# Performance work log

Hardware: AMD Instinct MI355X
Metric: run time of the kernel (lower is better)

The kernel has to match this reference:

```python
import jax, jax.numpy as jnp
import numpy as np

N = 50000
E = 800000
IN_CH, CDK, EDGE_DIM = 40, 200, 10
HID, HEADS = 64, 4
NEG_SLOPE = 0.2
SM_EPS = 1e-16
BN_EPS = 1e-5


def _glorot(key, shape):
    fan = shape[0] + shape[-1]
    return jax.random.normal(key, shape, jnp.float32) * jnp.sqrt(2.0 / fan)


def setup_inputs() -> dict:
    key = jax.random.key(0)
    ks = iter(jax.random.split(key, 40))
    inp = {
        'x': jax.random.normal(next(ks), (N, IN_CH), jnp.float32),
        'cdk_desc': jax.random.normal(next(ks), (N, CDK), jnp.float32),
        'edge_src': jax.random.randint(next(ks), (E,), 0, N, jnp.int32),
        'edge_dst': jax.random.randint(next(ks), (E,), 0, N, jnp.int32),
        'edge_attr': jax.random.normal(next(ks), (E, EDGE_DIM), jnp.float32),
    }
    dims = [(IN_CH + CDK, HEADS, HID), (HID * HEADS, HEADS, HID), (HID * HEADS, 1, HID)]
    for i, (din, h, c) in enumerate(dims):
        inp[f'W{i}'] = _glorot(next(ks), (din, h * c))
        inp[f'as{i}'] = _glorot(next(ks), (h, c))
        inp[f'ad{i}'] = _glorot(next(ks), (h, c))
        inp[f'We{i}'] = _glorot(next(ks), (EDGE_DIM, h * c))
        inp[f'ae{i}'] = _glorot(next(ks), (h, c))
        inp[f'b{i}'] = jnp.zeros((h * c,), jnp.float32)
        inp[f'g{i}'] = jnp.ones((h * c,), jnp.float32)
        inp[f'be{i}'] = jnp.zeros((h * c,), jnp.float32)
    inp['linW'] = _glorot(next(ks), (HID, 1))
    inp['linB'] = jnp.zeros((1,), jnp.float32)
    return inp


def gat_conv(x, src, dst, ea, W, a_s, a_d, We, a_e, b, heads, c):
    # PyG GATConv: shared linear for src/dst, edge features, segment softmax.
    xp = (x @ W).reshape(N, heads, c)                 # [N,H,C]
    ep = (ea @ We).reshape(-1, heads, c)              # [Etot,H,C]
    al_s = (xp * a_s).sum(-1)                         # [N,H]
    al_d = (xp * a_d).sum(-1)                         # [N,H]
    al_e = (ep * a_e).sum(-1)                         # [Etot,H]
    alpha = jax.nn.leaky_relu(al_s[src] + al_d[dst] + al_e, NEG_SLOPE)
    m = jax.ops.segment_max(alpha, dst, num_segments=N)
    ex = jnp.exp(alpha - m[dst])
    den = jax.ops.segment_sum(ex, dst, num_segments=N)
    att = ex / (den[dst] + SM_EPS)                    # [Etot,H]
    out = jax.ops.segment_sum(xp[src] * att[:, :, None], dst, num_segments=N)
    return out.reshape(N, heads * c) + b


def batch_norm(x, g, be):
    mu = x.mean(0)
    var = x.var(0)
    return g * (x - mu) * jax.lax.rsqrt(var + BN_EPS) + be


def reference(x, cdk_desc, edge_src, edge_dst, edge_attr,
              W0, as0, ad0, We0, ae0, b0, g0, be0,
              W1, as1, ad1, We1, ae1, b1, g1, be1,
              W2, as2, ad2, We2, ae2, b2, g2, be2,
              linW, linB):
    # add self-loops once (PyG default add_self_loops=True, fill_value='mean')
    loop = jnp.arange(N, dtype=edge_src.dtype)
    src = jnp.concatenate([edge_src, loop])
    dst = jnp.concatenate([edge_dst, loop])
    ea_mean = edge_attr.mean(0)
    ea = jnp.concatenate([edge_attr, jnp.broadcast_to(ea_mean, (N, EDGE_DIM))], 0)

    h = jnp.concatenate([x, cdk_desc], axis=-1)
    layers = [
        (W0, as0, ad0, We0, ae0, b0, g0, be0, HEADS),
        (W1, as1, ad1, We1, ae1, b1, g1, be1, HEADS),
        (W2, as2, ad2, We2, ae2, b2, g2, be2, 1),
    ]
    for (W, a_s, a_d, We, a_e, b, g, be, heads) in layers:
        h = gat_conv(h, src, dst, ea, W, a_s, a_d, We, a_e, b, heads, HID)
        h = batch_norm(h, g, be)
        h = jax.nn.elu(h)
        # dropout is identity in eval mode
    out = h @ linW + linB
    return jax.nn.sigmoid(out).squeeze(-1)
```

## Files before the change

### kernel.cpp

```cpp
#include <hip/hip_runtime.h>
#include <math.h>

#define NNODES 50000
#define NEDGES 800000
#define ETOT   (NNODES + NEDGES)
#define EDIM   10
#define SMEPS  1e-16f
#define BNEPS  1e-5f
#define NSLOPE 0.2f

#define SCANB  ((NNODES + 255) / 256)

typedef _Float16 f16;
typedef f16 f16x8 __attribute__((ext_vector_type(8)));
typedef f16 f16x4 __attribute__((ext_vector_type(4)));
typedef float f32x4 __attribute__((ext_vector_type(4)));


__global__ void k_deg(const int* __restrict__ edst, int* __restrict__ deg) {
    int e = blockIdx.x * blockDim.x + threadIdx.x;
    if (e >= ETOT) return;
    int d = (e < NEDGES) ? edst[e] : (e - NEDGES);
    atomicAdd(&deg[d], 1);
}

__global__ void k_scan1(const int* __restrict__ deg, int* __restrict__ off,
                        int* __restrict__ partials) {
    __shared__ int sm[256];
    int t = threadIdx.x;
    int i = blockIdx.x * 256 + t;
    int v = (i < NNODES) ? deg[i] : 0;
    sm[t] = v;
    __syncthreads();
    int val = v;
    for (int d = 1; d < 256; d <<= 1) {
        int tv = (t >= d) ? sm[t - d] : 0;
        __syncthreads();
        val += tv;
        sm[t] = val;
        __syncthreads();
    }
    if (i < NNODES) off[i] = val - v;
    if (t == 255) partials[blockIdx.x] = val;
}

__global__ void k_scan2(int* __restrict__ partials, int* __restrict__ off) {
    __shared__ int sm[256];
    int t = threadIdx.x;
    int v = (t < SCANB) ? partials[t] : 0;
    sm[t] = v;
    __syncthreads();
    int val = v;
    for (int d = 1; d < 256; d <<= 1) {
        int tv = (t >= d) ? sm[t - d] : 0;
        __syncthreads();
        val += tv;
        sm[t] = val;
        __syncthreads();
    }
    if (t < SCANB) partials[t] = val - v;
    if (t == 255) off[NNODES] = ETOT;
}

__global__ void k_scan3(int* __restrict__ off, const int* __restrict__ partials) {
    int i = blockIdx.x * 256 + threadIdx.x;
    if (i < NNODES) off[i] += partials[blockIdx.x];
}

__global__ void k_scatter(const int* __restrict__ esrc, const int* __restrict__ edst,
                          const int* __restrict__ off, int* __restrict__ cursor,
                          int* __restrict__ csr_src, int* __restrict__ perm) {
    int e = blockIdx.x * blockDim.x + threadIdx.x;
    if (e >= ETOT) return;
    int s, d;
    if (e < NEDGES) { s = esrc[e]; d = edst[e]; }
    else            { s = d = e - NEDGES; }
    int pos  = atomicAdd(&cursor[d], 1);
    int slot = off[d] + pos;
    csr_src[slot] = s;
    perm[e] = slot;
}

__global__ void k_easum(const float* __restrict__ ea, float* __restrict__ easum) {
    float acc[EDIM];
#pragma unroll
    for (int d = 0; d < EDIM; ++d) acc[d] = 0.f;
    for (int r = blockIdx.x * blockDim.x + threadIdx.x; r < NEDGES;
         r += gridDim.x * blockDim.x) {
#pragma unroll
        for (int d = 0; d < EDIM; ++d) acc[d] += ea[r * EDIM + d];
    }
    __shared__ float sm[256];
    for (int d = 0; d < EDIM; ++d) {
        sm[threadIdx.x] = acc[d];
        __syncthreads();
        for (int s = 128; s > 0; s >>= 1) {
            if (threadIdx.x < s) sm[threadIdx.x] += sm[threadIdx.x + s];
            __syncthreads();
        }
        if (threadIdx.x == 0) atomicAdd(&easum[d], sm[0]);
        __syncthreads();
    }
}

__global__ void k_concat_h(const float* __restrict__ x, const float* __restrict__ cdk,
                           f16* __restrict__ out) {
    int i = blockIdx.x * blockDim.x + threadIdx.x;
    if (i >= NNODES * 256) return;
    int n = i >> 8, j = i & 255;
    float v = (j < 40) ? x[n * 40 + j] : (j < 240) ? cdk[n * 200 + (j - 40)] : 0.f;
    out[i] = (f16)v;
}

__global__ void k_wcvt(const float* __restrict__ W, f16* __restrict__ Wt,
                       int K, int NC) {
    int i = blockIdx.x * blockDim.x + threadIdx.x;
    if (i >= NC * 256) return;
    int n = i >> 8, k = i & 255;
    Wt[i] = (k < K) ? (f16)W[k * NC + n] : (f16)0.f;
}

#define GM_LDS 40
__global__ __launch_bounds__(256) void k_gemm_h(const f16* __restrict__ A,
                                                const f16* __restrict__ Bt,
                                                f16* __restrict__ C,
                                                int M, int NC) {
    __shared__ f16 As[128 * GM_LDS];
    __shared__ f16 Bs[64 * GM_LDS];
    const int t    = threadIdx.x;
    const int w    = t >> 6;
    const int lane = t & 63;
    const int row0 = blockIdx.x * 128;
    const int col0 = blockIdx.y * 64;

    const int ar = t >> 1;
    const int ak = (t & 1) * 16;
    const int bn = t >> 2;
    const int bk = (t & 3) * 8;

    const int l16 = lane & 15;
    const int kg  = lane >> 4;

    f32x4 acc[2][4];
#pragma unroll
    for (int i = 0; i < 2; ++i)
#pragma unroll
        for (int j = 0; j < 4; ++j) acc[i][j] = {0.f, 0.f, 0.f, 0.f};

    for (int k0 = 0; k0 < 256; k0 += 32) {
        f16x8 av0, av1;
#pragma unroll
        for (int i = 0; i < 8; ++i) { av0[i] = (f16)0.f; av1[i] = (f16)0.f; }
        if (row0 + ar < M) {
            const f16* ap = &A[(long)(row0 + ar) * 256 + k0 + ak];
            av0 = *(const f16x8*)ap;
            av1 = *(const f16x8*)(ap + 8);
        }
        *(f16x8*)&As[ar * GM_LDS + ak]     = av0;
        *(f16x8*)&As[ar * GM_LDS + ak + 8] = av1;
        f16x8 bv = *(const f16x8*)&Bt[(long)(col0 + bn) * 256 + k0 + bk];
        *(f16x8*)&Bs[bn * GM_LDS + bk] = bv;
        __syncthreads();

        f16x8 afr[2], bfr[4];
#pragma unroll
        for (int mi = 0; mi < 2; ++mi)
            afr[mi] = *(const f16x8*)&As[(w * 32 + mi * 16 + l16) * GM_LDS + kg * 8];
#pragma unroll
        for (int ni = 0; ni < 4; ++ni)
            bfr[ni] = *(const f16x8*)&Bs[(ni * 16 + l16) * GM_LDS + kg * 8];
#pragma unroll
        for (int mi = 0; mi < 2; ++mi)
#pragma unroll
            for (int ni = 0; ni < 4; ++ni)
                acc[mi][ni] = __builtin_amdgcn_mfma_f32_16x16x32_f16(
                    afr[mi], bfr[ni], acc[mi][ni], 0, 0, 0);
        __syncthreads();
    }
#pragma unroll
    for (int mi = 0; mi < 2; ++mi)
#pragma unroll
        for (int ni = 0; ni < 4; ++ni)
#pragma unroll
            for (int j = 0; j < 4; ++j) {
                int r = row0 + w * 32 + mi * 16 + kg * 4 + j;
                if (r < M) C[(long)r * NC + col0 + ni * 16 + l16] = (f16)acc[mi][ni][j];
            }
}

template <int H>
__global__ __launch_bounds__(256) void k_attn_node(const f16* __restrict__ xp,
                                                   const float* __restrict__ a_s,
                                                   const float* __restrict__ a_d,
                                                   float* __restrict__ als,
                                                   float* __restrict__ ald) {
    int gw   = (blockIdx.x * blockDim.x + threadIdx.x) >> 6;
    int lane = threadIdx.x & 63;
    if (gw >= NNODES) return;
    if constexpr (H == 4) {
        int h = lane >> 4, c4 = (lane & 15) * 4;
        f16x4 xh = *(const f16x4*)&xp[(long)gw * 256 + lane * 4];
        float4 xv = make_float4((float)xh[0], (float)xh[1], (float)xh[2], (float)xh[3]);
        float4 ws = *(const float4*)&a_s[h * 64 + c4];
        float4 wd = *(const float4*)&a_d[h * 64 + c4];
        float ps = xv.x * ws.x + xv.y * ws.y + xv.z * ws.z + xv.w * ws.w;
        float pd = xv.x * wd.x + xv.y * wd.y + xv.z * wd.z + xv.w * wd.w;
        for (int o = 1; o < 16; o <<= 1) { ps += __shfl_xor(ps, o); pd += __shfl_xor(pd, o); }
        if ((lane & 15) == 0) { als[gw * 4 + h] = ps; ald[gw * 4 + h] = pd; }
    } else {
        float xv = (float)xp[(long)gw * 64 + lane];
        float ps = xv * a_s[lane];
        float pd = xv * a_d[lane];
        for (int o = 1; o < 64; o <<= 1) { ps += __shfl_xor(ps, o); pd += __shfl_xor(pd, o); }
        if (lane == 0) { als[gw] = ps; ald[gw] = pd; }
    }
}

__global__ void k_ve_all(const float* __restrict__ We0, const float* __restrict__ ae0,
                         const float* __restrict__ We1, const float* __restrict__ ae1,
                         const float* __restrict__ We2, const float* __restrict__ ae2,
                         const float* __restrict__ easum,
                         float* __restrict__ VeAll, float* __restrict__ laAll) {
    int l = blockIdx.x;
    const float* We = (l == 0) ? We0 : (l == 1) ? We1 : We2;
    const float* ae = (l == 0) ? ae0 : (l == 1) ? ae1 : ae2;
    int H = (l == 2) ? 1 : 4;
    float* Ve = VeAll + l * 48;
    float* la = laAll + l * 4;
    int t = threadIdx.x;
    if (t < EDIM * H) {
        int d = t / H, h = t % H;
        float s = 0.f;
        for (int c = 0; c < 64; ++c) s += We[d * (H * 64) + h * 64 + c] * ae[h * 64 + c];
        Ve[d * H + h] = s;
    }
    __syncthreads();
    if (t < H) {
        float s = 0.f;
        for (int d = 0; d < EDIM; ++d) s += (easum[d] * (1.0f / NEDGES)) * Ve[d * H + t];
        la[t] = s;
    }
}

template <int H>
__global__ void k_edge(const float* __restrict__ ea, const int* __restrict__ esrc,
                       const int* __restrict__ edst, const float* __restrict__ als,
                       const float* __restrict__ ald, const float* __restrict__ Ve,
                       const float* __restrict__ loop_al, const int* __restrict__ perm,
                       float* __restrict__ alpha) {
    int e = blockIdx.x * blockDim.x + threadIdx.x;
    if (e >= ETOT) return;
    int s, d;
    float ale[H];
    if (e < NEDGES) {
        s = esrc[e]; d = edst[e];
#pragma unroll
        for (int h = 0; h < H; ++h) ale[h] = 0.f;
#pragma unroll
        for (int dd = 0; dd < EDIM; ++dd) {
            float v = ea[(long)e * EDIM + dd];
#pragma unroll
            for (int h = 0; h < H; ++h) ale[h] = fmaf(v, Ve[dd * H + h], ale[h]);
        }
    } else {
        s = d = e - NEDGES;
#pragma unroll
        for (int h = 0; h < H; ++h) ale[h] = loop_al[h];
    }
    int slot = perm[e];
#pragma unroll
    for (int h = 0; h < H; ++h) {
        float a = als[s * H + h] + ald[d * H + h] + ale[h];
        a = (a > 0.f) ? a : NSLOPE * a;
        alpha[(long)slot * H + h] = a;
    }
}

template <int H>
__global__ __launch_bounds__(256) void k_agg(const f16* __restrict__ xp,
                                             const float* __restrict__ alpha,
                                             const int* __restrict__ off,
                                             const int* __restrict__ csr_src,
                                             float* __restrict__ out) {
    int gw   = (blockIdx.x * blockDim.x + threadIdx.x) >> 6;
    int lane = threadIdx.x & 63;
    if (gw >= NNODES) return;
    int o0 = off[gw], o1 = off[gw + 1];

    if constexpr (H == 4) {
        constexpr int T = 4;
        int h  = lane >> 4;
        int il = lane & 15;
        int glane = lane & 48;

        float av[T];
        int   idx[T];
        float mx = -INFINITY;
#pragma unroll
        for (int t = 0; t < T; ++t) {
            int s = o0 + t * 16 + il;
            bool ok = (s < o1);
            float a = ok ? alpha[(long)s * 4 + h] : -INFINITY;
            idx[t] = ok ? csr_src[s] : 0;
            av[t] = a;
            mx = fmaxf(mx, a);
        }
        for (int s = o0 + T * 16 + il; s < o1; s += 16)
            mx = fmaxf(mx, alpha[(long)s * 4 + h]);
#pragma unroll
        for (int o = 1; o < 16; o <<= 1) mx = fmaxf(mx, __shfl_xor(mx, o));

        float den = 0.f;
#pragma unroll
        for (int t = 0; t < T; ++t) {
            float e = expf(av[t] - mx);
            av[t] = e;
            den += e;
        }
        for (int s = o0 + T * 16 + il; s < o1; s += 16)
            den += expf(alpha[(long)s * 4 + h] - mx);
#pragma unroll
        for (int o = 1; o < 16; o <<= 1) den += __shfl_xor(den, o);
        float di = 1.0f / (den + SMEPS);

        float4 acc0 = make_float4(0.f, 0.f, 0.f, 0.f);
        float4 acc1 = make_float4(0.f, 0.f, 0.f, 0.f);
#pragma unroll
        for (int t = 0; t < T; ++t) {
            int base = o0 + t * 16;
            if (base >= o1) break;
            int cnt = min(16, o1 - base);
            int j = 0;
            for (; j + 4 <= cnt; j += 4) {
                float w0 = __shfl(av[t],  glane + j,     64);
                int  sn0 = __shfl(idx[t], glane + j,     64);
                float w1 = __shfl(av[t],  glane + j + 1, 64);
                int  sn1 = __shfl(idx[t], glane + j + 1, 64);
                float w2 = __shfl(av[t],  glane + j + 2, 64);
                int  sn2 = __shfl(idx[t], glane + j + 2, 64);
                float w3 = __shfl(av[t],  glane + j + 3, 64);
                int  sn3 = __shfl(idx[t], glane + j + 3, 64);
                f16x4 x0 = *(const f16x4*)&xp[(long)sn0 * 256 + lane * 4];
                f16x4 x1 = *(const f16x4*)&xp[(long)sn1 * 256 + lane * 4];
                f16x4 x2 = *(const f16x4*)&xp[(long)sn2 * 256 + lane * 4];
                f16x4 x3 = *(const f16x4*)&xp[(long)sn3 * 256 + lane * 4];
                acc0.x = fmaf(w0, (float)x0[0], acc0.x);
                acc0.y = fmaf(w0, (float)x0[1], acc0.y);
                acc0.z = fmaf(w0, (float)x0[2], acc0.z);
                acc0.w = fmaf(w0, (float)x0[3], acc0.w);
                acc1.x = fmaf(w1, (float)x1[0], acc1.x);
                acc1.y = fmaf(w1, (float)x1[1], acc1.y);
                acc1.z = fmaf(w1, (float)x1[2], acc1.z);
                acc1.w = fmaf(w1, (float)x1[3], acc1.w);
                acc0.x = fmaf(w2, (float)x2[0], acc0.x);
                acc0.y = fmaf(w2, (float)x2[1], acc0.y);
                acc0.z = fmaf(w2, (float)x2[2], acc0.z);
                acc0.w = fmaf(w2, (float)x2[3], acc0.w);
                acc1.x = fmaf(w3, (float)x3[0], acc1.x);
                acc1.y = fmaf(w3, (float)x3[1], acc1.y);
                acc1.z = fmaf(w3, (float)x3[2], acc1.z);
                acc1.w = fmaf(w3, (float)x3[3], acc1.w);
            }
            for (; j < cnt; ++j) {
                float w  = __shfl(av[t],  glane + j, 64);
                int   sn = __shfl(idx[t], glane + j, 64);
                f16x4 xh = *(const f16x4*)&xp[(long)sn * 256 + lane * 4];
                acc0.x = fmaf(w, (float)xh[0], acc0.x);
                acc0.y = fmaf(w, (float)xh[1], acc0.y);
                acc0.z = fmaf(w, (float)xh[2], acc0.z);
                acc0.w = fmaf(w, (float)xh[3], acc0.w);
            }
        }
        for (int s = o0 + T * 16; s < o1; ++s) {
            float w  = expf(alpha[(long)s * 4 + h] - mx);
            int   sn = csr_src[s];
            f16x4 xh = *(const f16x4*)&xp[(long)sn * 256 + lane * 4];
            acc0.x = fmaf(w, (float)xh[0], acc0.x);
            acc0.y = fmaf(w, (float)xh[1], acc0.y);
            acc0.z = fmaf(w, (float)xh[2], acc0.z);
            acc0.w = fmaf(w, (float)xh[3], acc0.w);
        }
        float4 acc = make_float4((acc0.x + acc1.x) * di, (acc0.y + acc1.y) * di,
                                 (acc0.z + acc1.z) * di, (acc0.w + acc1.w) * di);
        *(float4*)&out[(long)gw * 256 + lane * 4] = acc;
    } else {
        constexpr int T = 2;
        float av[T];
        int   idx[T];
        float mx = -INFINITY;
#pragma unroll
        for (int t = 0; t < T; ++t) {
            int s = o0 + t * 64 + lane;
            bool ok = (s < o1);
            float a = ok ? alpha[s] : -INFINITY;
            idx[t] = ok ? csr_src[s] : 0;
            av[t] = a;
            mx = fmaxf(mx, a);
        }
        for (int s = o0 + T * 64 + lane; s < o1; s += 64)
            mx = fmaxf(mx, alpha[s]);
#pragma unroll
        for (int o = 1; o < 64; o <<= 1) mx = fmaxf(mx, __shfl_xor(mx, o));

        float den = 0.f;
#pragma unroll
        for (int t = 0; t < T; ++t) {
            float e = expf(av[t] - mx);
            av[t] = e;
            den += e;
        }
        for (int s = o0 + T * 64 + lane; s < o1; s += 64)
            den += expf(alpha[s] - mx);
#pragma unroll
        for (int o = 1; o < 64; o <<= 1) den += __shfl_xor(den, o);
        float di = 1.0f / (den + SMEPS);

        float acc0 = 0.f, acc1 = 0.f;
#pragma unroll
        for (int t = 0; t < T; ++t) {
            int base = o0 + t * 64;
            if (base >= o1) break;
            int cnt = min(64, o1 - base);
            int j = 0;
            for (; j + 4 <= cnt; j += 4) {
                float w0 = __shfl(av[t],  j,     64);
                int  sn0 = __shfl(idx[t], j,     64);
                float w1 = __shfl(av[t],  j + 1, 64);
                int  sn1 = __shfl(idx[t], j + 1, 64);
                float w2 = __shfl(av[t],  j + 2, 64);
                int  sn2 = __shfl(idx[t], j + 2, 64);
                float w3 = __shfl(av[t],  j + 3, 64);
                int  sn3 = __shfl(idx[t], j + 3, 64);
                float x0 = (float)xp[(long)sn0 * 64 + lane];
                float x1 = (float)xp[(long)sn1 * 64 + lane];
                float x2 = (float)xp[(long)sn2 * 64 + lane];
                float x3 = (float)xp[(long)sn3 * 64 + lane];
                acc0 = fmaf(w0, x0, acc0);
                acc1 = fmaf(w1, x1, acc1);
                acc0 = fmaf(w2, x2, acc0);
                acc1 = fmaf(w3, x3, acc1);
            }
            for (; j < cnt; ++j) {
                float w  = __shfl(av[t],  j, 64);
                int   sn = __shfl(idx[t], j, 64);
                acc0 = fmaf(w, (float)xp[(long)sn * 64 + lane], acc0);
            }
        }
        for (int s = o0 + T * 64; s < o1; ++s) {
            float w  = expf(alpha[s] - mx);
            int   sn = csr_src[s];
            acc0 = fmaf(w, (float)xp[(long)sn * 64 + lane], acc0);
        }
        out[(long)gw * 64 + lane] = (acc0 + acc1) * di;
    }
}

__global__ void k_bnstats(const float* __restrict__ x, int width,
                          float* __restrict__ s1, float* __restrict__ s2) {
    int col  = threadIdx.x % width;
    int rsub = threadIdx.x / width;
    int rpb  = 256 / width;
    float a = 0.f, b = 0.f;
    for (int r = blockIdx.x * rpb + rsub; r < NNODES; r += gridDim.x * rpb) {
        float v = x[(long)r * width + col];
        a += v; b += v * v;
    }
    atomicAdd(&s1[col], a);
    atomicAdd(&s2[col], b);
}

__global__ void k_bnfin(const float* __restrict__ s1, const float* __restrict__ s2,
                        const float* __restrict__ g, const float* __restrict__ be,
                        int width, float* __restrict__ scale, float* __restrict__ shift) {
    int c = blockIdx.x * blockDim.x + threadIdx.x;
    if (c >= width) return;
    float mu  = s1[c] * (1.0f / NNODES);
    float var = s2[c] * (1.0f / NNODES) - mu * mu;
    float sc  = g[c] * rsqrtf(var + BNEPS);
    scale[c] = sc;
    shift[c] = be[c] - mu * sc;
}

__global__ void k_bnelu_h(const float* __restrict__ xin, f16* __restrict__ xout,
                          const float* __restrict__ scale, const float* __restrict__ shift,
                          int width) {
    long i = (long)(blockIdx.x * blockDim.x + threadIdx.x);
    long total = (long)NNODES * width;
    if (i * 4 >= total) return;
    float4 v = *(const float4*)&xin[i * 4];
    int c = (int)((i * 4) % width);
    float4 sc = *(const float4*)&scale[c];
    float4 sh = *(const float4*)&shift[c];
    float y0 = v.x * sc.x + sh.x;
    float y1 = v.y * sc.y + sh.y;
    float y2 = v.z * sc.z + sh.z;
    float y3 = v.w * sc.w + sh.w;
    y0 = (y0 > 0.f) ? y0 : expm1f(y0);
    y1 = (y1 > 0.f) ? y1 : expm1f(y1);
    y2 = (y2 > 0.f) ? y2 : expm1f(y2);
    y3 = (y3 > 0.f) ? y3 : expm1f(y3);
    f16x4 o = {(f16)y0, (f16)y1, (f16)y2, (f16)y3};
    *(f16x4*)&xout[i * 4] = o;
}

__global__ __launch_bounds__(256) void k_final(const f16* __restrict__ h,
                                               const float* __restrict__ linW,
                                               const float* __restrict__ linB,
                                               float* __restrict__ out) {
    int gw   = (blockIdx.x * blockDim.x + threadIdx.x) >> 6;
    int lane = threadIdx.x & 63;
    if (gw >= NNODES) return;
    float v = (float)h[(long)gw * 64 + lane] * linW[lane];
    for (int o = 32; o > 0; o >>= 1) v += __shfl_xor(v, o);
    if (lane == 0) out[gw] = 1.0f / (1.0f + expf(-(v + linB[0])));
}

extern "C" void kernel_launch(void* const* d_in, const int* in_sizes, int n_in,
                              void* d_out, int out_size, void* d_ws, size_t ws_size,
                              hipStream_t stream) {
    (void)in_sizes; (void)n_in; (void)out_size; (void)ws_size;
    const float* x    = (const float*)d_in[0];
    const float* cdk  = (const float*)d_in[1];
    const int*   esrc = (const int*)d_in[2];
    const int*   edst = (const int*)d_in[3];
    const float* ea   = (const float*)d_in[4];
    const float* W[3]   = {(const float*)d_in[5],  (const float*)d_in[13], (const float*)d_in[21]};
    const float* as_[3] = {(const float*)d_in[6],  (const float*)d_in[14], (const float*)d_in[22]};
    const float* ad_[3] = {(const float*)d_in[7],  (const float*)d_in[15], (const float*)d_in[23]};
    const float* We_[3] = {(const float*)d_in[8],  (const float*)d_in[16], (const float*)d_in[24]};
    const float* ae_[3] = {(const float*)d_in[9],  (const float*)d_in[17], (const float*)d_in[25]};
    const float* g_[3]  = {(const float*)d_in[11], (const float*)d_in[19], (const float*)d_in[27]};
    const float* be_[3] = {(const float*)d_in[12], (const float*)d_in[20], (const float*)d_in[28]};
    const float* linW = (const float*)d_in[29];
    const float* linB = (const float*)d_in[30];
    float* out = (float*)d_out;

    char* base = (char*)d_ws;
    size_t p = 0;
    auto alloc = [&](size_t bytes) -> void* {
        void* r = base + p;
        p = (p + bytes + 255) & ~(size_t)255;
        return r;
    };
    int*   deg     = (int*)alloc((size_t)NNODES * 4);
    int*   cursor  = (int*)alloc((size_t)NNODES * 4);
    float* easum   = (float*)alloc(EDIM * 4);
    float* s1a     = (float*)alloc((size_t)3 * 256 * 4);
    float* s2a     = (float*)alloc((size_t)3 * 256 * 4);
    size_t zero_bytes = p;
    int*   off     = (int*)alloc((size_t)(NNODES + 1) * 4);
    int*   partials= (int*)alloc((size_t)SCANB * 4);
    int*   csr_src = (int*)alloc((size_t)ETOT * 4);
    int*   perm    = (int*)alloc((size_t)ETOT * 4);
    float* alpha   = (float*)alloc((size_t)ETOT * 4 * 4);
    float* als     = (float*)alloc((size_t)NNODES * 4 * 4);
    float* ald     = (float*)alloc((size_t)NNODES * 4 * 4);
    float* VeAll   = (float*)alloc((size_t)3 * 48 * 4);
    float* laAll   = (float*)alloc((size_t)3 * 4 * 4);
    float* scale   = (float*)alloc(256 * 4);
    float* shift   = (float*)alloc(256 * 4);
    f16*   Wt[3];
    Wt[0]          = (f16*)alloc((size_t)256 * 256 * 2);
    Wt[1]          = (f16*)alloc((size_t)256 * 256 * 2);
    Wt[2]          = (f16*)alloc((size_t)64 * 256 * 2);
    f16*   bufA_h  = (f16*)alloc((size_t)NNODES * 256 * 2);
    f16*   bufXp_h = (f16*)alloc((size_t)NNODES * 256 * 2);
    float* bufC    = (float*)alloc((size_t)NNODES * 256 * 4);

    hipMemsetAsync(base, 0, zero_bytes, stream);

    int eb = (ETOT + 255) / 256;
    k_deg<<<eb, 256, 0, stream>>>(edst, deg);
    k_scan1<<<SCANB, 256, 0, stream>>>(deg, off, partials);
    k_scan2<<<1, 256, 0, stream>>>(partials, off);
    k_scan3<<<SCANB, 256, 0, stream>>>(off, partials);
    k_scatter<<<eb, 256, 0, stream>>>(esrc, edst, off, cursor, csr_src, perm);
    k_easum<<<256, 256, 0, stream>>>(ea, easum);
    k_concat_h<<<(NNODES * 256 + 255) / 256, 256, 0, stream>>>(x, cdk, bufA_h);
    k_wcvt<<<256, 256, 0, stream>>>(W[0], Wt[0], 240, 256);
    k_wcvt<<<256, 256, 0, stream>>>(W[1], Wt[1], 256, 256);
    k_wcvt<<<64,  256, 0, stream>>>(W[2], Wt[2], 256, 64);
    k_ve_all<<<3, 64, 0, stream>>>(We_[0], ae_[0], We_[1], ae_[1], We_[2], ae_[2],
                                   easum, VeAll, laAll);

    const int nodeblocks = (NNODES * 64) / 256;
    const int mblocks = (NNODES + 127) / 128;

    for (int l = 0; l < 3; ++l) {
        const int H  = (l == 2) ? 1 : 4;
        const int NC = H * 64;
        const float* Ve  = VeAll + l * 48;
        const float* la  = laAll + l * 4;
        float* s1 = s1a + l * 256;
        float* s2 = s2a + l * 256;
        dim3 gg(mblocks, NC / 64);
        k_gemm_h<<<gg, 256, 0, stream>>>(bufA_h, Wt[l], bufXp_h, NNODES, NC);
        if (H == 4) {
            k_attn_node<4><<<nodeblocks, 256, 0, stream>>>(bufXp_h, as_[l], ad_[l], als, ald);
            k_edge<4><<<eb, 256, 0, stream>>>(ea, esrc, edst, als, ald, Ve, la, perm, alpha);
            k_agg<4><<<nodeblocks, 256, 0, stream>>>(bufXp_h, alpha, off, csr_src, bufC);
        } else {
            k_attn_node<1><<<nodeblocks, 256, 0, stream>>>(bufXp_h, as_[l], ad_[l], als, ald);
            k_edge<1><<<eb, 256, 0, stream>>>(ea, esrc, edst, als, ald, Ve, la, perm, alpha);
            k_agg<1><<<nodeblocks, 256, 0, stream>>>(bufXp_h, alpha, off, csr_src, bufC);
        }
        k_bnstats<<<256, 256, 0, stream>>>(bufC, NC, s1, s2);
        k_bnfin<<<1, 256, 0, stream>>>(s1, s2, g_[l], be_[l], NC, scale, shift);
        k_bnelu_h<<<(NNODES * NC / 4 + 255) / 256, 256, 0, stream>>>(bufC, bufA_h, scale, shift, NC);
    }
    k_final<<<nodeblocks, 256, 0, stream>>>(bufA_h, linW, linB, out);
}
```

Before: 674.8 us.

## Store aggregation output in fp16, widen agg gathers, merge prep kernels

```diff
diff --git a/kernel.cpp b/kernel.cpp
--- a/kernel.cpp
+++ b/kernel.cpp
@@ -17,11 +17,32 @@
 typedef float f32x4 __attribute__((ext_vector_type(4)));
 
 
-__global__ void k_deg(const int* __restrict__ edst, int* __restrict__ deg) {
-    int e = blockIdx.x * blockDim.x + threadIdx.x;
-    if (e >= ETOT) return;
-    int d = (e < NEDGES) ? edst[e] : (e - NEDGES);
-    atomicAdd(&deg[d], 1);
+__global__ void k_edgeprep(const int* __restrict__ edst, int* __restrict__ deg,
+                           const float* __restrict__ ea, float* __restrict__ easum) {
+    int tid    = blockIdx.x * blockDim.x + threadIdx.x;
+    int stride = gridDim.x * blockDim.x;
+    for (int e = tid; e < ETOT; e += stride) {
+        int d = (e < NEDGES) ? edst[e] : (e - NEDGES);
+        atomicAdd(&deg[d], 1);
+    }
+    float acc[EDIM];
+#pragma unroll
+    for (int d = 0; d < EDIM; ++d) acc[d] = 0.f;
+    for (int r = tid; r < NEDGES; r += stride) {
+#pragma unroll
+        for (int d = 0; d < EDIM; ++d) acc[d] += ea[r * EDIM + d];
+    }
+    __shared__ float sm[256];
+    for (int d = 0; d < EDIM; ++d) {
+        sm[threadIdx.x] = acc[d];
+        __syncthreads();
+        for (int s = 128; s > 0; s >>= 1) {
+            if (threadIdx.x < s) sm[threadIdx.x] += sm[threadIdx.x + s];
+            __syncthreads();
+        }
+        if (threadIdx.x == 0) atomicAdd(&easum[d], sm[0]);
+        __syncthreads();
+    }
 }
 
 __global__ void k_scan1(const int* __restrict__ deg, int* __restrict__ off,
@@ -81,28 +102,6 @@
     perm[e] = slot;
 }
 
-__global__ void k_easum(const float* __restrict__ ea, float* __restrict__ easum) {
-    float acc[EDIM];
-#pragma unroll
-    for (int d = 0; d < EDIM; ++d) acc[d] = 0.f;
-    for (int r = blockIdx.x * blockDim.x + threadIdx.x; r < NEDGES;
-         r += gridDim.x * blockDim.x) {
-#pragma unroll
-        for (int d = 0; d < EDIM; ++d) acc[d] += ea[r * EDIM + d];
-    }
-    __shared__ float sm[256];
-    for (int d = 0; d < EDIM; ++d) {
-        sm[threadIdx.x] = acc[d];
-        __syncthreads();
-        for (int s = 128; s > 0; s >>= 1) {
-            if (threadIdx.x < s) sm[threadIdx.x] += sm[threadIdx.x + s];
-            __syncthreads();
-        }
-        if (threadIdx.x == 0) atomicAdd(&easum[d], sm[0]);
-        __syncthreads();
-    }
-}
-
 __global__ void k_concat_h(const float* __restrict__ x, const float* __restrict__ cdk,
                            f16* __restrict__ out) {
     int i = blockIdx.x * blockDim.x + threadIdx.x;
@@ -112,12 +111,17 @@
     out[i] = (f16)v;
 }
 
-__global__ void k_wcvt(const float* __restrict__ W, f16* __restrict__ Wt,
-                       int K, int NC) {
+__global__ void k_wcvt_all(const float* __restrict__ W0, const float* __restrict__ W1,
+                           const float* __restrict__ W2, f16* __restrict__ Wt0,
+                           f16* __restrict__ Wt1, f16* __restrict__ Wt2) {
     int i = blockIdx.x * blockDim.x + threadIdx.x;
-    if (i >= NC * 256) return;
-    int n = i >> 8, k = i & 255;
-    Wt[i] = (k < K) ? (f16)W[k * NC + n] : (f16)0.f;
+    const float* W; f16* Wt; int K, NC, j;
+    if (i < 65536)       { W = W0; Wt = Wt0; K = 240; NC = 256; j = i; }
+    else if (i < 131072) { W = W1; Wt = Wt1; K = 256; NC = 256; j = i - 65536; }
+    else if (i < 147456) { W = W2; Wt = Wt2; K = 256; NC = 64;  j = i - 131072; }
+    else return;
+    int n = j >> 8, k = j & 255;
+    Wt[j] = (k < K) ? (f16)W[k * NC + n] : (f16)0.f;
 }
 
 #define GM_LDS 40
@@ -281,17 +285,17 @@
                                              const float* __restrict__ alpha,
                                              const int* __restrict__ off,
                                              const int* __restrict__ csr_src,
-                                             float* __restrict__ out) {
+                                             f16* __restrict__ out) {
     int gw   = (blockIdx.x * blockDim.x + threadIdx.x) >> 6;
     int lane = threadIdx.x & 63;
     if (gw >= NNODES) return;
     int o0 = off[gw], o1 = off[gw + 1];
+    int cnt = o1 - o0;
 
     if constexpr (H == 4) {
         constexpr int T = 4;
         int h  = lane >> 4;
         int il = lane & 15;
-        int glane = lane & 48;
 
         float av[T];
         int   idx[T];
@@ -323,66 +327,78 @@
         for (int o = 1; o < 16; o <<= 1) den += __shfl_xor(den, o);
         float di = 1.0f / (den + SMEPS);
 
-        float4 acc0 = make_float4(0.f, 0.f, 0.f, 0.f);
-        float4 acc1 = make_float4(0.f, 0.f, 0.f, 0.f);
-#pragma unroll
-        for (int t = 0; t < T; ++t) {
-            int base = o0 + t * 16;
-            if (base >= o1) break;
-            int cnt = min(16, o1 - base);
-            int j = 0;
-            for (; j + 4 <= cnt; j += 4) {
-                float w0 = __shfl(av[t],  glane + j,     64);
-                int  sn0 = __shfl(idx[t], glane + j,     64);
-                float w1 = __shfl(av[t],  glane + j + 1, 64);
-                int  sn1 = __shfl(idx[t], glane + j + 1, 64);
-                float w2 = __shfl(av[t],  glane + j + 2, 64);
-                int  sn2 = __shfl(idx[t], glane + j + 2, 64);
-                float w3 = __shfl(av[t],  glane + j + 3, 64);
-                int  sn3 = __shfl(idx[t], glane + j + 3, 64);
-                f16x4 x0 = *(const f16x4*)&xp[(long)sn0 * 256 + lane * 4];
-                f16x4 x1 = *(const f16x4*)&xp[(long)sn1 * 256 + lane * 4];
-                f16x4 x2 = *(const f16x4*)&xp[(long)sn2 * 256 + lane * 4];
-                f16x4 x3 = *(const f16x4*)&xp[(long)sn3 * 256 + lane * 4];
-                acc0.x = fmaf(w0, (float)x0[0], acc0.x);
-                acc0.y = fmaf(w0, (float)x0[1], acc0.y);
-                acc0.z = fmaf(w0, (float)x0[2], acc0.z);
-                acc0.w = fmaf(w0, (float)x0[3], acc0.w);
-                acc1.x = fmaf(w1, (float)x1[0], acc1.x);
-                acc1.y = fmaf(w1, (float)x1[1], acc1.y);
-                acc1.z = fmaf(w1, (float)x1[2], acc1.z);
-                acc1.w = fmaf(w1, (float)x1[3], acc1.w);
-                acc0.x = fmaf(w2, (float)x2[0], acc0.x);
-                acc0.y = fmaf(w2, (float)x2[1], acc0.y);
-                acc0.z = fmaf(w2, (float)x2[2], acc0.z);
-                acc0.w = fmaf(w2, (float)x2[3], acc0.w);
-                acc1.x = fmaf(w3, (float)x3[0], acc1.x);
-                acc1.y = fmaf(w3, (float)x3[1], acc1.y);
-                acc1.z = fmaf(w3, (float)x3[2], acc1.z);
-                acc1.w = fmaf(w3, (float)x3[3], acc1.w);
+        if (cnt <= T * 16) {
+            int half = lane >> 5;
+            int ci   = lane & 31;
+            int hb   = (ci >> 3) << 4;
+            float a0[8], a1[8];
+#pragma unroll
+            for (int k = 0; k < 8; ++k) { a0[k] = 0.f; a1[k] = 0.f; }
+
+#pragma unroll
+            for (int t = 0; t < T; ++t) {
+                int base = t * 16;
+                if (base >= cnt) break;
+                int lim = min(16, cnt - base);
+                int jj = 0;
+                for (; jj + 8 <= lim; jj += 8) {
+                    int m0 = jj + half, m1 = jj + 2 + half;
+                    int m2 = jj + 4 + half, m3 = jj + 6 + half;
+                    float w0 = __shfl(av[t], hb | m0, 64);
+                    int  sn0 = __shfl(idx[t], m0, 64);
+                    float w1 = __shfl(av[t], hb | m1, 64);
+                    int  sn1 = __shfl(idx[t], m1, 64);
+                    float w2 = __shfl(av[t], hb | m2, 64);
+                    int  sn2 = __shfl(idx[t], m2, 64);
+                    float w3 = __shfl(av[t], hb | m3, 64);
+                    int  sn3 = __shfl(idx[t], m3, 64);
+                    f16x8 x0 = *(const f16x8*)&xp[(long)sn0 * 256 + ci * 8];
+                    f16x8 x1 = *(const f16x8*)&xp[(long)sn1 * 256 + ci * 8];
+                    f16x8 x2 = *(const f16x8*)&xp[(long)sn2 * 256 + ci * 8];
+                    f16x8 x3 = *(const f16x8*)&xp[(long)sn3 * 256 + ci * 8];
+#pragma unroll
+                    for (int k = 0; k < 8; ++k) {
+                        a0[k] = fmaf(w0, (float)x0[k], a0[k]);
+                        a1[k] = fmaf(w1, (float)x1[k], a1[k]);
+                        a0[k] = fmaf(w2, (float)x2[k], a0[k]);
+                        a1[k] = fmaf(w3, (float)x3[k], a1[k]);
+                    }
+                }
+                for (; jj < lim; jj += 2) {
+                    int m = jj + half;
+                    float w = __shfl(av[t], hb | (m & 15), 64);
+                    int  sn = __shfl(idx[t], m & 15, 64);
+                    f16x8 xv = *(const f16x8*)&xp[(long)sn * 256 + ci * 8];
+#pragma unroll
+                    for (int k = 0; k < 8; ++k)
+                        a0[k] = fmaf(w, (float)xv[k], a0[k]);
+                }
             }
-            for (; j < cnt; ++j) {
-                float w  = __shfl(av[t],  glane + j, 64);
-                int   sn = __shfl(idx[t], glane + j, 64);
-                f16x4 xh = *(const f16x4*)&xp[(long)sn * 256 + lane * 4];
-                acc0.x = fmaf(w, (float)xh[0], acc0.x);
-                acc0.y = fmaf(w, (float)xh[1], acc0.y);
-                acc0.z = fmaf(w, (float)xh[2], acc0.z);
-                acc0.w = fmaf(w, (float)xh[3], acc0.w);
+            float di_h = __shfl(di, (ci >> 3) << 4, 64);
+            f16x8 o;
+#pragma unroll
+            for (int k = 0; k < 8; ++k) {
+                float v = a0[k] + a1[k];
+                v += __shfl_xor(v, 32);
+                o[k] = (f16)(v * di_h);
             }
-        }
-        for (int s = o0 + T * 16; s < o1; ++s) {
-            float w  = expf(alpha[(long)s * 4 + h] - mx);
-            int   sn = csr_src[s];
-            f16x4 xh = *(const f16x4*)&xp[(long)sn * 256 + lane * 4];
-            acc0.x = fmaf(w, (float)xh[0], acc0.x);
-            acc0.y = fmaf(w, (float)xh[1], acc0.y);
-            acc0.z = fmaf(w, (float)xh[2], acc0.z);
-            acc0.w = fmaf(w, (float)xh[3], acc0.w);
-        }
-        float4 acc = make_float4((acc0.x + acc1.x) * di, (acc0.y + acc1.y) * di,
-                                 (acc0.z + acc1.z) * di, (acc0.w + acc1.w) * di);
-        *(float4*)&out[(long)gw * 256 + lane * 4] = acc;
+            if (half == 0)
+                *(f16x8*)&out[(long)gw * 256 + ci * 8] = o;
+        } else {
+            float4 acc = make_float4(0.f, 0.f, 0.f, 0.f);
+            for (int s = o0; s < o1; ++s) {
+                float w  = expf(alpha[(long)s * 4 + h] - mx);
+                int   sn = csr_src[s];
+                f16x4 xv = *(const f16x4*)&xp[(long)sn * 256 + lane * 4];
+                acc.x = fmaf(w, (float)xv[0], acc.x);
+                acc.y = fmaf(w, (float)xv[1], acc.y);
+                acc.z = fmaf(w, (float)xv[2], acc.z);
+                acc.w = fmaf(w, (float)xv[3], acc.w);
+            }
+            f16x4 o4 = {(f16)(acc.x * di), (f16)(acc.y * di),
+                        (f16)(acc.z * di), (f16)(acc.w * di)};
+            *(f16x4*)&out[(long)gw * 256 + lane * 4] = o4;
+        }
     } else {
         constexpr int T = 2;
         float av[T];
@@ -420,9 +436,9 @@
         for (int t = 0; t < T; ++t) {
             int base = o0 + t * 64;
             if (base >= o1) break;
-            int cnt = min(64, o1 - base);
+            int c2 = min(64, o1 - base);
             int j = 0;
-            for (; j + 4 <= cnt; j += 4) {
+            for (; j + 4 <= c2; j += 4) {
                 float w0 = __shfl(av[t],  j,     64);
                 int  sn0 = __shfl(idx[t], j,     64);
                 float w1 = __shfl(av[t],  j + 1, 64);
@@ -440,7 +456,7 @@
                 acc0 = fmaf(w2, x2, acc0);
                 acc1 = fmaf(w3, x3, acc1);
             }
-            for (; j < cnt; ++j) {
+            for (; j < c2; ++j) {
                 float w  = __shfl(av[t],  j, 64);
                 int   sn = __shfl(idx[t], j, 64);
                 acc0 = fmaf(w, (float)xp[(long)sn * 64 + lane], acc0);
@@ -451,18 +467,18 @@
             int   sn = csr_src[s];
             acc0 = fmaf(w, (float)xp[(long)sn * 64 + lane], acc0);
         }
-        out[(long)gw * 64 + lane] = (acc0 + acc1) * di;
-    }
-}
-
-__global__ void k_bnstats(const float* __restrict__ x, int width,
+        out[(long)gw * 64 + lane] = (f16)((acc0 + acc1) * di);
+    }
+}
+
+__global__ void k_bnstats(const f16* __restrict__ x, int width,
                           float* __restrict__ s1, float* __restrict__ s2) {
     int col  = threadIdx.x % width;
     int rsub = threadIdx.x / width;
     int rpb  = 256 / width;
     float a = 0.f, b = 0.f;
     for (int r = blockIdx.x * rpb + rsub; r < NNODES; r += gridDim.x * rpb) {
-        float v = x[(long)r * width + col];
+        float v = (float)x[(long)r * width + col];
         a += v; b += v * v;
     }
     atomicAdd(&s1[col], a);
@@ -481,20 +497,20 @@
     shift[c] = be[c] - mu * sc;
 }
 
-__global__ void k_bnelu_h(const float* __restrict__ xin, f16* __restrict__ xout,
+__global__ void k_bnelu_h(const f16* __restrict__ xin, f16* __restrict__ xout,
                           const float* __restrict__ scale, const float* __restrict__ shift,
                           int width) {
     long i = (long)(blockIdx.x * blockDim.x + threadIdx.x);
     long total = (long)NNODES * width;
     if (i * 4 >= total) return;
-    float4 v = *(const float4*)&xin[i * 4];
+    f16x4 v4 = *(const f16x4*)&xin[i * 4];
     int c = (int)((i * 4) % width);
     float4 sc = *(const float4*)&scale[c];
     float4 sh = *(const float4*)&shift[c];
-    float y0 = v.x * sc.x + sh.x;
-    float y1 = v.y * sc.y + sh.y;
-    float y2 = v.z * sc.z + sh.z;
-    float y3 = v.w * sc.w + sh.w;
+    float y0 = (float)v4[0] * sc.x + sh.x;
+    float y1 = (float)v4[1] * sc.y + sh.y;
+    float y2 = (float)v4[2] * sc.z + sh.z;
+    float y3 = (float)v4[3] * sc.w + sh.w;
     y0 = (y0 > 0.f) ? y0 : expm1f(y0);
     y1 = (y1 > 0.f) ? y1 : expm1f(y1);
     y2 = (y2 > 0.f) ? y2 : expm1f(y2);
@@ -565,21 +581,18 @@
     Wt[2]          = (f16*)alloc((size_t)64 * 256 * 2);
     f16*   bufA_h  = (f16*)alloc((size_t)NNODES * 256 * 2);
     f16*   bufXp_h = (f16*)alloc((size_t)NNODES * 256 * 2);
-    float* bufC    = (float*)alloc((size_t)NNODES * 256 * 4);
+    f16*   bufC_h  = (f16*)alloc((size_t)NNODES * 256 * 2);
 
     hipMemsetAsync(base, 0, zero_bytes, stream);
 
     int eb = (ETOT + 255) / 256;
-    k_deg<<<eb, 256, 0, stream>>>(edst, deg);
+    k_edgeprep<<<256, 256, 0, stream>>>(edst, deg, ea, easum);
     k_scan1<<<SCANB, 256, 0, stream>>>(deg, off, partials);
     k_scan2<<<1, 256, 0, stream>>>(partials, off);
     k_scan3<<<SCANB, 256, 0, stream>>>(off, partials);
     k_scatter<<<eb, 256, 0, stream>>>(esrc, edst, off, cursor, csr_src, perm);
-    k_easum<<<256, 256, 0, stream>>>(ea, easum);
     k_concat_h<<<(NNODES * 256 + 255) / 256, 256, 0, stream>>>(x, cdk, bufA_h);
-    k_wcvt<<<256, 256, 0, stream>>>(W[0], Wt[0], 240, 256);
-    k_wcvt<<<256, 256, 0, stream>>>(W[1], Wt[1], 256, 256);
-    k_wcvt<<<64,  256, 0, stream>>>(W[2], Wt[2], 256, 64);
+    k_wcvt_all<<<576, 256, 0, stream>>>(W[0], W[1], W[2], Wt[0], Wt[1], Wt[2]);
     k_ve_all<<<3, 64, 0, stream>>>(We_[0], ae_[0], We_[1], ae_[1], We_[2], ae_[2],
                                    easum, VeAll, laAll);
 
@@ -598,15 +611,15 @@
         if (H == 4) {
             k_attn_node<4><<<nodeblocks, 256, 0, stream>>>(bufXp_h, as_[l], ad_[l], als, ald);
             k_edge<4><<<eb, 256, 0, stream>>>(ea, esrc, edst, als, ald, Ve, la, perm, alpha);
-            k_agg<4><<<nodeblocks, 256, 0, stream>>>(bufXp_h, alpha, off, csr_src, bufC);
+            k_agg<4><<<nodeblocks, 256, 0, stream>>>(bufXp_h, alpha, off, csr_src, bufC_h);
         } else {
             k_attn_node<1><<<nodeblocks, 256, 0, stream>>>(bufXp_h, as_[l], ad_[l], als, ald);
             k_edge<1><<<eb, 256, 0, stream>>>(ea, esrc, edst, als, ald, Ve, la, perm, alpha);
-            k_agg<1><<<nodeblocks, 256, 0, stream>>>(bufXp_h, alpha, off, csr_src, bufC);
-        }
-        k_bnstats<<<256, 256, 0, stream>>>(bufC, NC, s1, s2);
+            k_agg<1><<<nodeblocks, 256, 0, stream>>>(bufXp_h, alpha, off, csr_src, bufC_h);
+        }
+        k_bnstats<<<256, 256, 0, stream>>>(bufC_h, NC, s1, s2);
         k_bnfin<<<1, 256, 0, stream>>>(s1, s2, g_[l], be_[l], NC, scale, shift);
-        k_bnelu_h<<<(NNODES * NC / 4 + 255) / 256, 256, 0, stream>>>(bufC, bufA_h, scale, shift, NC);
+        k_bnelu_h<<<(NNODES * NC / 4 + 255) / 256, 256, 0, stream>>>(bufC_h, bufA_h, scale, shift, NC);
     }
     k_final<<<nodeblocks, 256, 0, stream>>>(bufA_h, linW, linB, out);
 }
```

Measured after the change: 646.6 us (median of 2 runs). 1.04x faster.
